# Optimization experiments

Measured on AMD Instinct MI355X. Metric: run time of the kernel, lower is better.

## Reference

```python
import jax, jax.numpy as jnp
from jax import lax
import numpy as np

UNTIL_T = 25  # until_time in source
EPS = 1e-6
K_SEG = 5     # number of temporal groups produced by Segment()


def conv1d(x, w, b=None, padding=((0, 0),)):
    y = lax.conv_general_dilated(x, w, (1,), padding,
                                 dimension_numbers=('NCH', 'OIH', 'NCH'))
    return y if b is None else y + b[None, :, None]


def maxpool1d(x, k, s):
    return lax.reduce_window(x, -jnp.inf, lax.max, (1, 1, k), (1, 1, s), 'VALID')


def batchnorm(x, g, b):
    m = x.mean((0, 2), keepdims=True)
    v = x.var((0, 2), keepdims=True)
    return g[None, :, None] * (x - m) / jnp.sqrt(v + 1e-5) + b[None, :, None]


def miu(x, sign, a, b):
    # fuzzy membership predicate: sigmoid(sign * a_c * (x - b_c))
    return jax.nn.sigmoid(sign * a[None, :, None] * (x - b[None, :, None]))


def upsample2(x):
    B, C, L = x.shape
    return jax.image.resize(x, (B, C, 2 * L), method='linear')


def logic_and(x, w, padding=((0, 0),)):
    # weighted geometric-mean fuzzy AND: exp(conv(log x, softmax(w)))
    wn = jax.nn.softmax(w.reshape(w.shape[0], -1), -1).reshape(w.shape)
    return jax.nn.relu(jnp.exp(conv1d(jnp.log(jnp.clip(x, 0.0, 1.0) + EPS), wn, padding=padding)))


def logic_or(x, w, padding=((0, 0),)):
    # dual fuzzy OR: 1 - exp(conv(log(1-x), softmax(w)))
    wn = jax.nn.softmax(w.reshape(w.shape[0], -1), -1).reshape(w.shape)
    return jax.nn.relu(1.0 - jnp.exp(conv1d(jnp.log(1.0 - jnp.clip(x, 0.0, 1.0) + EPS), wn, padding=padding)))


def until(x, T):
    # Until(x)[t] = max_{1<=d<=T} min( min_{0<=s<d} x[t+s], x[t+d] ), zero right-pad
    L = x.shape[-1]
    xp = jnp.pad(x, ((0, 0), (0, 0), (0, T)))
    runmin = x
    out = jnp.zeros_like(x)  # x >= 0 so 0 is a valid lower bound
    for d in range(1, T + 1):  # small fixed unroll over until_time
        xs = xp[..., d:d + L]
        out = jnp.maximum(out, jnp.minimum(runmin, xs))
        runmin = jnp.minimum(runmin, xs)
    return out[..., :L - 1]  # crop to match kernel-2 logic convs


def forward(x, wave_w, bn_g, bn_b, miu_ap, miu_bp, miu_an, miu_bn,
            ae_w1, ae_b1, ae_w2, ae_b2, ae_w3, ae_b3, ae_w4, ae_b4,
            and2_w, or2_w, and_w, or_w,
            fc1_w, fc1_b, fc2_w, fc2_b, fc3_w, fc3_b):
    B = x.shape[0]
    # Basic predicate network: wavelet conv (k=32) + BN + ReLU + pool -> [B,16,343]
    xf = maxpool1d(jax.nn.relu(batchnorm(conv1d(x, wave_w), bn_g, bn_b)), 3, 2)
    x_pos = maxpool1d(miu(xf, 1.0, miu_ap, miu_bp), 3, 2)    # [B,16,171]
    x_neg = maxpool1d(miu(xf, -1.0, miu_an, miu_bn), 3, 2)   # [B,16,171]
    x_miu = jnp.concatenate([x_pos, x_neg], 1)               # [B,32,171]
    # AutoEncoder -> w, same shape as x_miu
    h = maxpool1d(jnp.tanh(conv1d(x_miu, ae_w1, ae_b1, ((1, 1),))), 3, 2)   # [B,64,85]
    h = maxpool1d(jax.nn.relu(conv1d(h, ae_w2, ae_b2, ((1, 1),))), 3, 2)    # [B,32,42]
    h = jnp.tanh(conv1d(upsample2(h), ae_w3, ae_b3, ((2, 2),)))             # [B,64,86]
    h = jax.nn.sigmoid(conv1d(upsample2(h), ae_w4, ae_b4, ((2, 2),)))       # [B,32,174]
    w = maxpool1d(h, 4, 1)                                                  # [B,32,171]
    # Temporal grouping: K_SEG activation-level bands over w (vectorized, no cat loop)
    lo = (jnp.arange(K_SEG, dtype=w.dtype) / K_SEG)[:, None, None, None]
    hi = (jnp.arange(1, K_SEG + 1, dtype=w.dtype) / K_SEG).at[-1].set(2.0)[:, None, None, None]
    masks = (w[None] >= lo) & (w[None] < hi)                 # [K,B,32,171]
    seg = jnp.where(masks, w[None], 0.0) * x_miu[None]       # select_w * x_miu per segment
    inp = jnp.transpose(seg, (1, 0, 2, 3)).reshape(B, K_SEG * 32, -1)  # [B,160,171]
    x_until = until(inp, UNTIL_T)                            # [B,160,170]
    x_and1 = logic_and(inp, and2_w)                          # [B,20,170]
    x_or1 = logic_or(inp, or2_w)                             # [B,20,170]
    x1 = jnp.concatenate([x_and1, x_or1, x_until], 1)        # [B,200,170]
    x_and2 = logic_and(x1, and_w, ((1, 0),))                 # causal same-pad -> [B,6,170]
    x_or2 = logic_or(x1, or_w, ((1, 0),))                    # [B,6,170]
    x2 = jnp.concatenate([x_and2, x_or2], 1)                 # [B,12,170]
    # Classifier (dropout = identity at inference), Linear over last dim (=170)
    h = jax.nn.relu(jnp.einsum('bcl,ol->bco', x2, fc1_w) + fc1_b)
    h = jax.nn.relu(jnp.einsum('bco,po->bcp', h, fc2_w) + fc2_b)
    return jnp.einsum('bcp,qp->bcq', h, fc3_w) + fc3_b       # [B,12,10]


def setup_inputs() -> dict:
    key = jax.random.key(0)
    ks = jax.random.split(key, 24)
    n = lambda k, shp, s: jax.random.normal(k, shp, jnp.float32) * s
    B = 128
    d = {
        'x': n(ks[0], (B, 1, 719), 1.0),
        'wave_w': n(ks[1], (16, 1, 32), 1.0 / np.sqrt(32)),
        'bn_g': jnp.ones((16,), jnp.float32),
        'bn_b': jnp.zeros((16,), jnp.float32),
        'miu_ap': 1.0 + n(ks[2], (16,), 0.1),
        'miu_bp': n(ks[3], (16,), 0.1),
        'miu_an': 1.0 + n(ks[4], (16,), 0.1),
        'miu_bn': n(ks[5], (16,), 0.1),
        'ae_w1': n(ks[6], (64, 32, 3), 1.0 / np.sqrt(96)),
        'ae_b1': jnp.zeros((64,), jnp.float32),
        'ae_w2': n(ks[7], (32, 64, 3), 1.0 / np.sqrt(192)),
        'ae_b2': jnp.zeros((32,), jnp.float32),
        'ae_w3': n(ks[8], (64, 32, 3), 1.0 / np.sqrt(96)),
        'ae_b3': jnp.zeros((64,), jnp.float32),
        'ae_w4': n(ks[9], (32, 64, 3), 1.0 / np.sqrt(192)),
        'ae_b4': jnp.zeros((32,), jnp.float32),
        'and2_w': n(ks[10], (20, 160, 2), 1.0),
        'or2_w': n(ks[11], (20, 160, 2), 1.0),
        'and_w': n(ks[12], (6, 200, 2), 1.0),
        'or_w': n(ks[13], (6, 200, 2), 1.0),
        'fc1_w': n(ks[14], (1024, 170), 1.0 / np.sqrt(170)),
        'fc1_b': jnp.zeros((1024,), jnp.float32),
        'fc2_w': n(ks[15], (256, 1024), 1.0 / np.sqrt(1024)),
        'fc2_b': jnp.zeros((256,), jnp.float32),
        'fc3_w': n(ks[16], (10, 256), 1.0 / np.sqrt(256)),
        'fc3_b': jnp.zeros((10,), jnp.float32),
    }
    return d


def reference(x, wave_w, bn_g, bn_b, miu_ap, miu_bp, miu_an, miu_bn,
              ae_w1, ae_b1, ae_w2, ae_b2, ae_w3, ae_b3, ae_w4, ae_b4,
              and2_w, or2_w, and_w, or_w,
              fc1_w, fc1_b, fc2_w, fc2_b, fc3_w, fc3_b):
    return forward(x, wave_w, bn_g, bn_b, miu_ap, miu_bp, miu_an, miu_bn,
                   ae_w1, ae_b1, ae_w2, ae_b2, ae_w3, ae_b3, ae_w4, ae_b4,
                   and2_w, or2_w, and_w, or_w,
                   fc1_w, fc1_b, fc2_w, fc2_b, fc3_w, fc3_b)
```

## Files before the change

### kernel.cpp

```cpp
#include <hip/hip_runtime.h>

#define TPB 256
static inline int cdiv(int a, int b){ return (a + b - 1) / b; }

#define EPSL 1e-6f
#define ACT_TANH 0
#define ACT_RELU 1
#define ACT_SIG  2
#define ACT_NONE 3

__device__ __forceinline__ float sigf(float x){ return 1.0f / (1.0f + __expf(-x)); }
__device__ __forceinline__ float clip01(float x){ return fminf(fmaxf(x, 0.f), 1.f); }

#define OFF_Y1   0
#define OFF_XF   1409024
#define OFF_XMIU 2111488
#define OFF_H1   2811904
#define OFF_INP  4384768
#define OFF_X1   7886848
#define OFF_TAIL 12238848
#define OFF_P1   0
#define OFF_P2   (OFF_INP + 400000)
#define OFF_GP   0
#define OFF_X2P  OFF_INP
#define OFF_FC1H OFF_X1
#define OFF_BNP  (OFF_TAIL + 64)
#define OFF_WN   (OFF_TAIL + 64 + 512)
#define OFF_W1P  (OFF_TAIL + 64 + 512 + 17600)

__global__ void __launch_bounds__(TPB) k_misc(const float* __restrict__ a2, const float* __restrict__ o2,
                     const float* __restrict__ aw, const float* __restrict__ ow,
                     float* __restrict__ wn,
                     const float* __restrict__ x, const float* __restrict__ ww,
                     float* __restrict__ y,
                     const float* __restrict__ w1, float* __restrict__ wp){
  int bid = blockIdx.x;
  if (bid < 52){
    const float* src; float* dst; int n;
    if (bid < 20)      { src = a2 + bid*320;      dst = wn + bid*320;              n = 320; }
    else if (bid < 40) { src = o2 + (bid-20)*320; dst = wn + 6400 + (bid-20)*320;  n = 320; }
    else if (bid < 46) { src = aw + (bid-40)*400; dst = wn + 12800 + (bid-40)*400; n = 400; }
    else               { src = ow + (bid-46)*400; dst = wn + 15200 + (bid-46)*400; n = 400; }
    __shared__ float sh[TPB];
    float m = -1e30f;
    for (int i = threadIdx.x; i < n; i += TPB) m = fmaxf(m, src[i]);
    sh[threadIdx.x] = m; __syncthreads();
    for (int off = TPB/2; off > 0; off >>= 1){
      if (threadIdx.x < off) sh[threadIdx.x] = fmaxf(sh[threadIdx.x], sh[threadIdx.x+off]);
      __syncthreads();
    }
    m = sh[0]; __syncthreads();
    float s = 0.f;
    for (int i = threadIdx.x; i < n; i += TPB) s += expf(src[i] - m);
    sh[threadIdx.x] = s; __syncthreads();
    for (int off = TPB/2; off > 0; off >>= 1){
      if (threadIdx.x < off) sh[threadIdx.x] += sh[threadIdx.x+off];
      __syncthreads();
    }
    float inv = 1.0f / sh[0];
    __syncthreads();
    for (int i = threadIdx.x; i < n; i += TPB) dst[i] = expf(src[i] - m) * inv;
  } else if (bid < 52 + 5504){
    int idx = (bid - 52)*TPB + threadIdx.x;
    int l = idx % 688; int t = idx / 688; int o = t & 15; int b = t >> 4;
    const float* xr = x + b*719 + l;
    const float* wr = ww + o*32;
    float s = 0.f;
    #pragma unroll
    for (int k = 0; k < 32; k++) s = fmaf(xr[k], wr[k], s);
    y[idx] = s;
  } else {
    int idx = (bid - 5556)*TPB + threadIdx.x;
    int k = idx % 192; int o = idx / 192;
    wp[idx] = (k < 170) ? w1[o*170 + k] : 0.f;
  }
}

__global__ void k_bn_part(const float* __restrict__ y, double* __restrict__ bnp){
  int c = blockIdx.x & 15, ch = blockIdx.x >> 4;
  double s = 0.0, s2 = 0.0;
  for (int i = threadIdx.x; i < 16*688; i += TPB){
    int b = ch*16 + i/688, l = i % 688;
    float v = y[(b*16 + c)*688 + l];
    s += (double)v; s2 += (double)v * (double)v;
  }
  __shared__ double sh[TPB], sh2[TPB];
  sh[threadIdx.x] = s; sh2[threadIdx.x] = s2; __syncthreads();
  for (int off = TPB/2; off > 0; off >>= 1){
    if (threadIdx.x < off){ sh[threadIdx.x] += sh[threadIdx.x+off]; sh2[threadIdx.x] += sh2[threadIdx.x+off]; }
    __syncthreads();
  }
  if (threadIdx.x == 0){ bnp[blockIdx.x] = sh[0]; bnp[128 + blockIdx.x] = sh2[0]; }
}

__global__ void k_xmiu2(const float* __restrict__ y, const double* __restrict__ bnp,
                        const float* __restrict__ g, const float* __restrict__ bb,
                        const float* __restrict__ ap, const float* __restrict__ bp,
                        const float* __restrict__ an, const float* __restrict__ bn,
                        float* __restrict__ out){
  __shared__ float smean[16], srstd[16];
  if (threadIdx.x < 16){
    int cc = threadIdx.x;
    double s = 0.0, s2 = 0.0;
    #pragma unroll
    for (int j = 0; j < 8; j++){ s += bnp[j*16 + cc]; s2 += bnp[128 + j*16 + cc]; }
    double n = 128.0*688.0;
    double m = s / n;
    double var = s2 / n - m*m;
    smean[cc] = (float)m;
    srstd[cc] = (float)(1.0 / sqrt(var + 1e-5));
  }
  __syncthreads();
  int idx = blockIdx.x*blockDim.x + threadIdx.x;
  if (idx >= 128*32*171) return;
  int l = idx % 171; int t = idx / 171; int c = t & 31; int b = t >> 5;
  int cc = c & 15;
  float mean = smean[cc], rstd = srstd[cc];
  float gc = g[cc], bc = bb[cc];
  float sign = (c < 16) ? 1.f : -1.f;
  float a  = (c < 16) ? ap[cc] : an[cc];
  float bo = (c < 16) ? bp[cc] : bn[cc];
  const float* yr = y + (b*16 + cc)*688 + 4*l;
  float v[7];
  #pragma unroll
  for (int i = 0; i < 7; i++)
    v[i] = fmaxf(fmaf(gc*(yr[i] - mean), rstd, bc), 0.f);
  float m = -1e30f;
  #pragma unroll
  for (int j = 0; j < 3; j++){
    float xf = fmaxf(fmaxf(v[2*j], v[2*j+1]), v[2*j+2]);
    m = fmaxf(m, sigf(sign * a * (xf - bo)));
  }
  out[idx] = m;
}

template<int SMODE, int LSRC, int LEFF>
__device__ __forceinline__ float stage_val(const float* __restrict__ src, int q){
  if (q < 0 || q >= LEFF) return 0.f;
  if constexpr (SMODE == 0){
    return src[q];
  } else if constexpr (SMODE == 1){
    float m = fmaxf(fmaxf(src[2*q], src[2*q+1]), src[2*q+2]);
    return tanhf(m);
  } else if constexpr (SMODE == 2){
    auto P = [&](int k){
      float m = fmaxf(fmaxf(src[2*k], src[2*k+1]), src[2*k+2]);
      return fmaxf(m, 0.f);
    };
    if (q == 0) return P(0);
    if (q == LEFF - 1) return P(LEFF/2 - 1);
    int k = q >> 1;
    return (q & 1) ? 0.75f*P(k) + 0.25f*P(k+1) : 0.25f*P(k-1) + 0.75f*P(k);
  } else {
    if (q == 0) return src[0];
    if (q == LEFF - 1) return src[LSRC - 1];
    int k = q >> 1;
    return (q & 1) ? 0.75f*src[k] + 0.25f*src[k+1] : 0.25f*src[k-1] + 0.75f*src[k];
  }
}

template<int CIN, int LSRC, int LEFF, int COUT, int LOUT, int PAD, int ACT, int PL, int SMODE>
__global__ void __launch_bounds__(256) k_conv(const float* __restrict__ in,
                                              const float* __restrict__ w,
                                              const float* __restrict__ bias,
                                              float* __restrict__ outp){
  constexpr int LSEG = 4*PL;
  constexpr int WL = ((LSEG + 2) + 3) & ~3;
  constexpr int K3 = CIN*3;
  __shared__ float smem[CIN*WL + 8 + K3*COUT];
  float* sin = smem;
  float* wT  = smem + CIN*WL + 8;
  const int b = blockIdx.x;
  const int tid = threadIdx.x;
  const int base = blockIdx.y*LSEG - PAD;

  const float* gin = in + b*CIN*LSRC;
  for (int e = tid; e < CIN*WL; e += 256){
    int i = e / WL, c = e - i*WL;
    sin[e] = stage_val<SMODE, LSRC, LEFF>(gin + i*LSRC, base + c);
  }
  if (tid < 8) sin[CIN*WL + tid] = 0.f;
  for (int e = tid; e < K3*COUT; e += 256){
    int o = e & (COUT-1), m = e / COUT;
    wT[m*COUT + o] = w[o*K3 + m];
  }
  __syncthreads();

  const int to = tid / PL, tp = tid - (tid/PL)*PL;
  const int o0 = to*4;
  const int pl0 = 4*tp;
  float acc[4][4] = {{0,0,0,0},{0,0,0,0},{0,0,0,0},{0,0,0,0}};

  for (int i = 0; i < CIN; i++){
    const float* srow = sin + i*WL + pl0;
    float xv[6];
    *(float4*)&xv[0] = *(const float4*)srow;
    *(float2*)&xv[4] = *(const float2*)(srow + 4);
    const float* wrow = wT + (i*3)*COUT + o0;
    float wv[3][4];
    #pragma unroll
    for (int k = 0; k < 3; k++)
      *(float4*)&wv[k][0] = *(const float4*)(wrow + k*COUT);
    #pragma unroll
    for (int j = 0; j < 4; j++)
      #pragma unroll
      for (int k = 0; k < 3; k++)
        #pragma unroll
        for (int oo = 0; oo < 4; oo++)
          acc[j][oo] = fmaf(xv[j+k], wv[k][oo], acc[j][oo]);
  }

  const int pg0 = blockIdx.y*LSEG + pl0;
  float bv[4];
  #pragma unroll
  for (int oo = 0; oo < 4; oo++) bv[oo] = bias[o0 + oo];
  #pragma unroll
  for (int oo = 0; oo < 4; oo++){
    float* orow = outp + (b*COUT + o0 + oo)*LOUT;
    #pragma unroll
    for (int j = 0; j < 4; j++){
      int p = pg0 + j;
      if (p < LOUT){
        float s = acc[j][oo] + bv[oo];
        float r;
        if (ACT == ACT_TANH)      r = tanhf(s);
        else if (ACT == ACT_RELU) r = fmaxf(s, 0.f);
        else if (ACT == ACT_SIG)  r = sigf(s);
        else                      r = s;
        orow[p] = r;
      }
    }
  }
}

__global__ void k_inp(const float* __restrict__ h4, const float* __restrict__ xmiu,
                      float* __restrict__ inp){
  int idx = blockIdx.x*blockDim.x + threadIdx.x;
  if (idx >= 128*32*171) return;
  int l = idx % 171; int t = idx / 171; int c = t & 31; int b = t >> 5;
  const float* hr = h4 + t*174 + l;
  float wv = fmaxf(fmaxf(hr[0], hr[1]), fmaxf(hr[2], hr[3]));
  float xm = xmiu[idx];
  float prod = wv * xm;
  const float lo[5] = {0.0f, 0.2f, 0.4f, 0.6f, 0.8f};
  const float hi[5] = {0.2f, 0.4f, 0.6f, 0.8f, 2.0f};
  float* op = inp + ((b*160) + c)*171 + l;
  #pragma unroll
  for (int s = 0; s < 5; s++){
    bool m = (wv >= lo[s]) && (wv < hi[s]);
    op[s*32*171] = m ? prod : 0.f;
  }
}

__global__ void __launch_bounds__(TPB) k_ul1(const float* __restrict__ inp, const float* __restrict__ wn,
                                             float* __restrict__ x1, float* __restrict__ p1){
  int bid = blockIdx.x;
  if (bid < 680){
    int xb = bid % 85; int rr = bid / 85; int ch = rr & 3; int v = rr >> 2;
    int bl = xb*TPB + threadIdx.x;
    int l = bl % 170; int b = bl / 170;
    const float* W = wn + (v ? 6400 : 0);
    float acc[20];
    #pragma unroll
    for (int o = 0; o < 20; o++) acc[o] = 0.f;
    int c0 = ch*40;
    const float* ir = inp + (b*160 + c0)*171 + l;
    for (int c = 0; c < 40; c++){
      float u0 = clip01(ir[0]);
      float u1 = clip01(ir[1]);
      float g0, g1;
      if (v){ g0 = __logf(1.f - u0 + EPSL); g1 = __logf(1.f - u1 + EPSL); }
      else  { g0 = __logf(u0 + EPSL);       g1 = __logf(u1 + EPSL); }
      const float* wc = W + 2*(c0 + c);
      #pragma unroll
      for (int o = 0; o < 20; o++)
        acc[o] = fmaf(wc[o*320], g0, fmaf(wc[o*320 + 1], g1, acc[o]));
      ir += 171;
    }
    float* pp = p1 + ((ch*128 + b)*40 + v*20)*170 + l;
    #pragma unroll
    for (int o = 0; o < 20; o++) pp[o*170] = acc[o];
  } else {
    int idx = (bid - 680)*TPB + threadIdx.x;
    int lh = idx % 85; int t = idx / 85; int c = t % 160; int b = t / 160;
    int l0 = 2*lh;
    const float* xr = inp + (b*160 + c)*171;
    float v[27];
    #pragma unroll
    for (int i = 0; i < 27; i++){
      int q = l0 + i;
      v[i] = (q < 171) ? xr[q] : 0.f;
    }
    float rm0 = v[0], o0 = 0.f;
    float rm1 = v[1], o1 = 0.f;
    #pragma unroll
    for (int d = 1; d <= 25; d++){
      o0 = fmaxf(o0, fminf(rm0, v[d]));     rm0 = fminf(rm0, v[d]);
      o1 = fmaxf(o1, fminf(rm1, v[d+1]));   rm1 = fminf(rm1, v[d+1]);
    }
    float2 ov = {o0, o1};
    *(float2*)&x1[((b*200) + 40 + c)*170 + l0] = ov;
  }
}

__global__ void __launch_bounds__(TPB) k_logic2p(const float* __restrict__ x1, const float* __restrict__ p1,
                                                 const float* __restrict__ wn, float* __restrict__ p2){
  int bl = blockIdx.x*TPB + threadIdx.x;
  int l = bl % 170; int b = bl / 170;
  int ch = blockIdx.y, v = blockIdx.z;
  const float* W = wn + 12800 + (v ? 2400 : 0);
  float acc[6] = {0.f,0.f,0.f,0.f,0.f,0.f};
  int c0 = ch*25;
  bool have0 = (l > 0);
  for (int c = c0; c < c0 + 25; c++){
    float u0 = 0.f, u1;
    if (c < 40){
      float s1 = 0.f;
      #pragma unroll
      for (int q = 0; q < 4; q++) s1 += p1[((q*128 + b)*40 + c)*170 + l];
      float e = __expf(s1);
      u1 = (c < 20) ? e : fmaxf(0.f, 1.f - e);
      if (have0){
        float s0 = 0.f;
        #pragma unroll
        for (int q = 0; q < 4; q++) s0 += p1[((q*128 + b)*40 + c)*170 + l - 1];
        float e0 = __expf(s0);
        u0 = (c < 20) ? e0 : fmaxf(0.f, 1.f - e0);
      }
    } else {
      const float* xr = x1 + (b*200 + c)*170 + l;
      u1 = xr[0];
      if (have0) u0 = xr[-1];
    }
    float g0 = 0.f;
    if (have0){
      float uc = clip01(u0);
      g0 = v ? __logf(1.f - uc + EPSL) : __logf(uc + EPSL);
    }
    float uc1 = clip01(u1);
    float g1 = v ? __logf(1.f - uc1 + EPSL) : __logf(uc1 + EPSL);
    const float* wc = W + 2*c;
    #pragma unroll
    for (int o = 0; o < 6; o++)
      acc[o] = fmaf(wc[o*400], g0, fmaf(wc[o*400 + 1], g1, acc[o]));
  }
  float* pp = p2 + ((ch*128 + b)*12 + v*6)*170 + l;
  #pragma unroll
  for (int o = 0; o < 6; o++) pp[o*170] = acc[o];
}

__global__ void k_fin2(const float* __restrict__ p2, float* __restrict__ x2p){
  int idx = blockIdx.x*blockDim.x + threadIdx.x;
  if (idx >= 128*12*192) return;
  int l = idx % 192; int ro = idx / 192;
  if (l >= 170){ x2p[ro*192 + l] = 0.f; return; }
  int o = ro % 12; int b = ro / 12;
  float s = 0.f;
  #pragma unroll
  for (int ch = 0; ch < 8; ch++) s += p2[((ch*128 + b)*12 + o)*170 + l];
  float e = __expf(s);
  float r = (o < 6) ? e : fmaxf(0.f, 1.f - e);
  x2p[ro*192 + l] = r;
}

template<int M, int N, int K, int KSPLIT, int ACT>
__global__ void __launch_bounds__(256) k_gemm(const float* __restrict__ A,
                                              const float* __restrict__ W,
                                              const float* __restrict__ bias,
                                              float* __restrict__ C){
  static_assert(K % (KSPLIT*32) == 0, "K split");
  constexpr int KC = K / KSPLIT;
  constexpr int NT = KC / 32;
  constexpr int S = 68;
  __shared__ float As[2][32*S];
  __shared__ float Bs[2][32*S];
  const int m0 = blockIdx.x*64, n0 = blockIdx.y*64;
  const int kbeg = blockIdx.z*KC;
  const int tid = threadIdx.x;
  const int row = tid >> 2;
  const int c4  = (tid & 3)*4;
  const int tm  = (tid & 15)*4;
  const int tn  = (tid >> 4)*4;

  const float* Ar = A + (m0 + row)*K + kbeg + c4;
  const float* Wr = W + (n0 + row)*K + kbeg + c4;

  float4 ra0 = *(const float4*)(Ar);
  float4 ra1 = *(const float4*)(Ar + 16);
  float4 rb0 = *(const float4*)(Wr);
  float4 rb1 = *(const float4*)(Wr + 16);

  float acc[4][4] = {{0,0,0,0},{0,0,0,0},{0,0,0,0},{0,0,0,0}};
  int buf = 0;
  {
    float* a = As[0]; float* b = Bs[0];
    #pragma unroll
    for (int i = 0; i < 4; i++){
      a[(c4 + i)*S + row]      = ((const float*)&ra0)[i];
      a[(c4 + 16 + i)*S + row] = ((const float*)&ra1)[i];
      b[(c4 + i)*S + row]      = ((const float*)&rb0)[i];
      b[(c4 + 16 + i)*S + row] = ((const float*)&rb1)[i];
    }
  }
  __syncthreads();

  for (int t = 0; t < NT; t++){
    if (t + 1 < NT){
      Ar += 32; Wr += 32;
      ra0 = *(const float4*)(Ar);
      ra1 = *(const float4*)(Ar + 16);
      rb0 = *(const float4*)(Wr);
      rb1 = *(const float4*)(Wr + 16);
    }
    const float* a = As[buf]; const float* b = Bs[buf];
    #pragma unroll
    for (int k = 0; k < 32; k++){
      const float4 av = *(const float4*)(a + k*S + tm);
      const float4 bv = *(const float4*)(b + k*S + tn);
      acc[0][0] = fmaf(av.x, bv.x, acc[0][0]); acc[0][1] = fmaf(av.x, bv.y, acc[0][1]);
      acc[0][2] = fmaf(av.x, bv.z, acc[0][2]); acc[0][3] = fmaf(av.x, bv.w, acc[0][3]);
      acc[1][0] = fmaf(av.y, bv.x, acc[1][0]); acc[1][1] = fmaf(av.y, bv.y, acc[1][1]);
      acc[1][2] = fmaf(av.y, bv.z, acc[1][2]); acc[1][3] = fmaf(av.y, bv.w, acc[1][3]);
      acc[2][0] = fmaf(av.z, bv.x, acc[2][0]); acc[2][1] = fmaf(av.z, bv.y, acc[2][1]);
      acc[2][2] = fmaf(av.z, bv.z, acc[2][2]); acc[2][3] = fmaf(av.z, bv.w, acc[2][3]);
      acc[3][0] = fmaf(av.w, bv.x, acc[3][0]); acc[3][1] = fmaf(av.w, bv.y, acc[3][1]);
      acc[3][2] = fmaf(av.w, bv.z, acc[3][2]); acc[3][3] = fmaf(av.w, bv.w, acc[3][3]);
    }
    if (t + 1 < NT){
      int nb = buf ^ 1;
      float* an = As[nb]; float* bn = Bs[nb];
      #pragma unroll
      for (int i = 0; i < 4; i++){
        an[(c4 + i)*S + row]      = ((const float*)&ra0)[i];
        an[(c4 + 16 + i)*S + row] = ((const float*)&ra1)[i];
        bn[(c4 + i)*S + row]      = ((const float*)&rb0)[i];
        bn[(c4 + 16 + i)*S + row] = ((const float*)&rb1)[i];
      }
      __syncthreads();
      buf = nb;
    }
  }

  if (KSPLIT == 1){
    #pragma unroll
    for (int i = 0; i < 4; i++){
      float4 vv;
      vv.x = acc[i][0] + bias[n0 + tn];
      vv.y = acc[i][1] + bias[n0 + tn + 1];
      vv.z = acc[i][2] + bias[n0 + tn + 2];
      vv.w = acc[i][3] + bias[n0 + tn + 3];
      if (ACT == ACT_RELU){
        vv.x = fmaxf(vv.x, 0.f); vv.y = fmaxf(vv.y, 0.f);
        vv.z = fmaxf(vv.z, 0.f); vv.w = fmaxf(vv.w, 0.f);
      }
      *(float4*)&C[(m0 + tm + i)*N + n0 + tn] = vv;
    }
  } else {
    float* Cz = C + (size_t)blockIdx.z*M*N;
    #pragma unroll
    for (int i = 0; i < 4; i++){
      float4 vv = {acc[i][0], acc[i][1], acc[i][2], acc[i][3]};
      *(float4*)&Cz[(m0 + tm + i)*N + n0 + tn] = vv;
    }
  }
}

__global__ void __launch_bounds__(256) k_tail(const float* __restrict__ gp,
                                              const float* __restrict__ b2,
                                              const float* __restrict__ w3,
                                              const float* __restrict__ b3,
                                              float* __restrict__ out){
  constexpr int MN = 1536*256;
  __shared__ float sh[256];
  __shared__ float ps[160];
  const int row = blockIdx.x;
  const int t = threadIdx.x;
  float s = b2[t];
  #pragma unroll
  for (int z = 0; z < 4; z++) s += gp[(size_t)z*MN + row*256 + t];
  sh[t] = fmaxf(s, 0.f);
  __syncthreads();
  if (t < 160){
    int q = t >> 4, j = t & 15;
    const float* wr = w3 + q*256 + j*16;
    const float* hr = sh + j*16;
    float p = 0.f;
    #pragma unroll
    for (int i = 0; i < 16; i++) p = fmaf(hr[i], wr[i], p);
    ps[t] = p;
  }
  __syncthreads();
  if (t < 10){
    float s3 = b3[t];
    #pragma unroll
    for (int j = 0; j < 16; j++) s3 += ps[t*16 + j];
    out[row*10 + t] = s3;
  }
}

extern "C" void kernel_launch(void* const* d_in, const int* in_sizes, int n_in,
                              void* d_out, int out_size, void* d_ws, size_t ws_size,
                              hipStream_t stream) {
  const float* x      = (const float*)d_in[0];
  const float* wave_w = (const float*)d_in[1];
  const float* bn_g   = (const float*)d_in[2];
  const float* bn_b   = (const float*)d_in[3];
  const float* miu_ap = (const float*)d_in[4];
  const float* miu_bp = (const float*)d_in[5];
  const float* miu_an = (const float*)d_in[6];
  const float* miu_bn = (const float*)d_in[7];
  const float* ae_w1  = (const float*)d_in[8];
  const float* ae_b1  = (const float*)d_in[9];
  const float* ae_w2  = (const float*)d_in[10];
  const float* ae_b2  = (const float*)d_in[11];
  const float* ae_w3  = (const float*)d_in[12];
  const float* ae_b3  = (const float*)d_in[13];
  const float* ae_w4  = (const float*)d_in[14];
  const float* ae_b4  = (const float*)d_in[15];
  const float* and2_w = (const float*)d_in[16];
  const float* or2_w  = (const float*)d_in[17];
  const float* and_w  = (const float*)d_in[18];
  const float* or_w   = (const float*)d_in[19];
  const float* fc1_w  = (const float*)d_in[20];
  const float* fc1_b  = (const float*)d_in[21];
  const float* fc2_w  = (const float*)d_in[22];
  const float* fc2_b  = (const float*)d_in[23];
  const float* fc3_w  = (const float*)d_in[24];
  const float* fc3_b  = (const float*)d_in[25];
  float* out = (float*)d_out;
  float* ws  = (float*)d_ws;

  float* y1    = ws + OFF_Y1;
  float* xmiu  = ws + OFF_XMIU;
  float* c1    = ws + OFF_H1;
  float* c2    = ws + OFF_XF;
  float* h3    = ws + OFF_Y1;
  float* h4    = ws + OFF_H1;
  float* inp   = ws + OFF_INP;
  float* x1    = ws + OFF_X1;
  float* p1    = ws + OFF_P1;
  float* p2    = ws + OFF_P2;
  float* gp    = ws + OFF_GP;
  float* x2p   = ws + OFF_X2P;
  float* w1p   = ws + OFF_W1P;
  float* fc1h  = ws + OFF_FC1H;
  double* bnp  = (double*)(ws + OFF_BNP);
  float* wn    = ws + OFF_WN;

  k_misc     <<<52 + 5504 + 768, TPB, 0, stream>>>(and2_w, or2_w, and_w, or_w, wn,
                                                   x, wave_w, y1, fc1_w, w1p);
  k_bn_part  <<<128, TPB, 0, stream>>>(y1, bnp);
  k_xmiu2    <<<cdiv(128*32*171, TPB), TPB, 0, stream>>>(y1, bnp, bn_g, bn_b,
                                                         miu_ap, miu_bp, miu_an, miu_bn, xmiu);

  k_conv<32,171,171,64,171,1,ACT_NONE,16,0><<<dim3(128,3), 256, 0, stream>>>(xmiu, ae_w1, ae_b1, c1);
  k_conv<64,171, 85,32, 85,1,ACT_NONE,32,1><<<dim3(128,1), 256, 0, stream>>>(c1, ae_w2, ae_b2, c2);
  k_conv<32, 85, 84,64, 86,2,ACT_TANH,16,2><<<dim3(128,2), 256, 0, stream>>>(c2, ae_w3, ae_b3, h3);
  k_conv<64, 86,172,32,174,2,ACT_SIG ,32,3><<<dim3(128,2), 256, 0, stream>>>(h3, ae_w4, ae_b4, h4);

  k_inp      <<<cdiv(128*32*171, TPB), TPB, 0, stream>>>(h4, xmiu, inp);
  k_ul1      <<<680 + 6800, TPB, 0, stream>>>(inp, wn, x1, p1);
  k_logic2p  <<<dim3(85, 8, 2), TPB, 0, stream>>>(x1, p1, wn, p2);
  k_fin2     <<<cdiv(128*12*192, TPB), TPB, 0, stream>>>(p2, x2p);

  k_gemm<1536,1024,192,1,ACT_RELU><<<dim3(24,16,1), 256, 0, stream>>>(x2p, w1p, fc1_b, fc1h);
  k_gemm<1536,256,1024,4,ACT_NONE><<<dim3(24,4,4), 256, 0, stream>>>(fc1h, fc2_w, fc2_b, gp);
  k_tail     <<<1536, 256, 0, stream>>>(gp, fc2_b, fc3_w, fc3_b, out);
}
```

Before: 317.2 us.

## Split reductions and conv tiles finer to raise grid parallelism across kernels

Doubles the block count for the batchnorm partial sums, and splits the fuzzy-AND/OR channel reduction into eight chunks instead of four, moving the p1 buffer to a new offset so it fits. Adds a per-thread output-tile template parameter to the conv kernel so the two 32-output-channel convs use 2-wide tiles with more blocks. Makes the until kernel compute four outputs per thread so the 25-step window loads are shared. The aim is better GPU occupancy for small grids, at the cost of more partial-sum traffic and scalar shared-memory loads in place of vector loads.

Result: faster. 297.7 us (-6.1%).

```diff
diff --git a/kernel.cpp b/kernel.cpp
--- a/kernel.cpp
+++ b/kernel.cpp
@@ -19,14 +19,14 @@
 #define OFF_INP  4384768
 #define OFF_X1   7886848
 #define OFF_TAIL 12238848
-#define OFF_P1   0
 #define OFF_P2   (OFF_INP + 400000)
 #define OFF_GP   0
 #define OFF_X2P  OFF_INP
 #define OFF_FC1H OFF_X1
 #define OFF_BNP  (OFF_TAIL + 64)
-#define OFF_WN   (OFF_TAIL + 64 + 512)
-#define OFF_W1P  (OFF_TAIL + 64 + 512 + 17600)
+#define OFF_WN   (OFF_TAIL + 64 + 1024)
+#define OFF_W1P  (OFF_TAIL + 64 + 1024 + 17600)
+#define OFF_P1   16000000
 
 __global__ void __launch_bounds__(TPB) k_misc(const float* __restrict__ a2, const float* __restrict__ o2,
                      const float* __restrict__ aw, const float* __restrict__ ow,
@@ -79,8 +79,8 @@
 __global__ void k_bn_part(const float* __restrict__ y, double* __restrict__ bnp){
   int c = blockIdx.x & 15, ch = blockIdx.x >> 4;
   double s = 0.0, s2 = 0.0;
-  for (int i = threadIdx.x; i < 16*688; i += TPB){
-    int b = ch*16 + i/688, l = i % 688;
+  for (int i = threadIdx.x; i < 8*688; i += TPB){
+    int b = ch*8 + i/688, l = i % 688;
     float v = y[(b*16 + c)*688 + l];
     s += (double)v; s2 += (double)v * (double)v;
   }
@@ -90,7 +90,7 @@
     if (threadIdx.x < off){ sh[threadIdx.x] += sh[threadIdx.x+off]; sh2[threadIdx.x] += sh2[threadIdx.x+off]; }
     __syncthreads();
   }
-  if (threadIdx.x == 0){ bnp[blockIdx.x] = sh[0]; bnp[128 + blockIdx.x] = sh2[0]; }
+  if (threadIdx.x == 0){ bnp[blockIdx.x] = sh[0]; bnp[256 + blockIdx.x] = sh2[0]; }
 }
 
 __global__ void k_xmiu2(const float* __restrict__ y, const double* __restrict__ bnp,
@@ -103,7 +103,7 @@
     int cc = threadIdx.x;
     double s = 0.0, s2 = 0.0;
     #pragma unroll
-    for (int j = 0; j < 8; j++){ s += bnp[j*16 + cc]; s2 += bnp[128 + j*16 + cc]; }
+    for (int j = 0; j < 16; j++){ s += bnp[j*16 + cc]; s2 += bnp[256 + j*16 + cc]; }
     double n = 128.0*688.0;
     double m = s / n;
     double var = s2 / n - m*m;
@@ -159,12 +159,12 @@
   }
 }
 
-template<int CIN, int LSRC, int LEFF, int COUT, int LOUT, int PAD, int ACT, int PL, int SMODE>
+template<int CIN, int LSRC, int LEFF, int COUT, int LOUT, int PAD, int ACT, int PL, int SMODE, int JT>
 __global__ void __launch_bounds__(256) k_conv(const float* __restrict__ in,
                                               const float* __restrict__ w,
                                               const float* __restrict__ bias,
                                               float* __restrict__ outp){
-  constexpr int LSEG = 4*PL;
+  constexpr int LSEG = JT*PL;
   constexpr int WL = ((LSEG + 2) + 3) & ~3;
   constexpr int K3 = CIN*3;
   __shared__ float smem[CIN*WL + 8 + K3*COUT];
@@ -188,21 +188,25 @@
 
   const int to = tid / PL, tp = tid - (tid/PL)*PL;
   const int o0 = to*4;
-  const int pl0 = 4*tp;
-  float acc[4][4] = {{0,0,0,0},{0,0,0,0},{0,0,0,0},{0,0,0,0}};
+  const int pl0 = JT*tp;
+  float acc[JT][4];
+  #pragma unroll
+  for (int j = 0; j < JT; j++)
+    #pragma unroll
+    for (int oo = 0; oo < 4; oo++) acc[j][oo] = 0.f;
 
   for (int i = 0; i < CIN; i++){
     const float* srow = sin + i*WL + pl0;
-    float xv[6];
-    *(float4*)&xv[0] = *(const float4*)srow;
-    *(float2*)&xv[4] = *(const float2*)(srow + 4);
+    float xv[JT+2];
+    #pragma unroll
+    for (int j = 0; j < JT+2; j++) xv[j] = srow[j];
     const float* wrow = wT + (i*3)*COUT + o0;
     float wv[3][4];
     #pragma unroll
     for (int k = 0; k < 3; k++)
       *(float4*)&wv[k][0] = *(const float4*)(wrow + k*COUT);
     #pragma unroll
-    for (int j = 0; j < 4; j++)
+    for (int j = 0; j < JT; j++)
       #pragma unroll
       for (int k = 0; k < 3; k++)
         #pragma unroll
@@ -218,7 +222,7 @@
   for (int oo = 0; oo < 4; oo++){
     float* orow = outp + (b*COUT + o0 + oo)*LOUT;
     #pragma unroll
-    for (int j = 0; j < 4; j++){
+    for (int j = 0; j < JT; j++){
       int p = pg0 + j;
       if (p < LOUT){
         float s = acc[j][oo] + bv[oo];
@@ -255,17 +259,17 @@
 __global__ void __launch_bounds__(TPB) k_ul1(const float* __restrict__ inp, const float* __restrict__ wn,
                                              float* __restrict__ x1, float* __restrict__ p1){
   int bid = blockIdx.x;
-  if (bid < 680){
-    int xb = bid % 85; int rr = bid / 85; int ch = rr & 3; int v = rr >> 2;
+  if (bid < 1360){
+    int xb = bid % 85; int rr = bid / 85; int ch = rr & 7; int v = rr >> 3;
     int bl = xb*TPB + threadIdx.x;
     int l = bl % 170; int b = bl / 170;
     const float* W = wn + (v ? 6400 : 0);
     float acc[20];
     #pragma unroll
     for (int o = 0; o < 20; o++) acc[o] = 0.f;
-    int c0 = ch*40;
+    int c0 = ch*20;
     const float* ir = inp + (b*160 + c0)*171 + l;
-    for (int c = 0; c < 40; c++){
+    for (int c = 0; c < 20; c++){
       float u0 = clip01(ir[0]);
       float u1 = clip01(ir[1]);
       float g0, g1;
@@ -281,25 +285,30 @@
     #pragma unroll
     for (int o = 0; o < 20; o++) pp[o*170] = acc[o];
   } else {
-    int idx = (bid - 680)*TPB + threadIdx.x;
-    int lh = idx % 85; int t = idx / 85; int c = t % 160; int b = t / 160;
-    int l0 = 2*lh;
+    int idx = (bid - 1360)*TPB + threadIdx.x;
+    int lh = idx % 43; int t = idx / 43; int c = t % 160; int b = t / 160;
+    int l0 = 4*lh;
     const float* xr = inp + (b*160 + c)*171;
-    float v[27];
-    #pragma unroll
-    for (int i = 0; i < 27; i++){
+    float v[29];
+    #pragma unroll
+    for (int i = 0; i < 29; i++){
       int q = l0 + i;
       v[i] = (q < 171) ? xr[q] : 0.f;
     }
     float rm0 = v[0], o0 = 0.f;
     float rm1 = v[1], o1 = 0.f;
+    float rm2 = v[2], o2 = 0.f;
+    float rm3 = v[3], o3 = 0.f;
     #pragma unroll
     for (int d = 1; d <= 25; d++){
       o0 = fmaxf(o0, fminf(rm0, v[d]));     rm0 = fminf(rm0, v[d]);
       o1 = fmaxf(o1, fminf(rm1, v[d+1]));   rm1 = fminf(rm1, v[d+1]);
-    }
-    float2 ov = {o0, o1};
-    *(float2*)&x1[((b*200) + 40 + c)*170 + l0] = ov;
+      o2 = fmaxf(o2, fminf(rm2, v[d+2]));   rm2 = fminf(rm2, v[d+2]);
+      o3 = fmaxf(o3, fminf(rm3, v[d+3]));   rm3 = fminf(rm3, v[d+3]);
+    }
+    float* xw = x1 + ((b*200) + 40 + c)*170;
+    if (l0 + 1 < 170){ float2 ov = {o0, o1}; *(float2*)&xw[l0] = ov; }
+    if (l0 + 3 < 170){ float2 ov = {o2, o3}; *(float2*)&xw[l0 + 2] = ov; }
   }
 }
 
@@ -317,13 +326,13 @@
     if (c < 40){
       float s1 = 0.f;
       #pragma unroll
-      for (int q = 0; q < 4; q++) s1 += p1[((q*128 + b)*40 + c)*170 + l];
+      for (int q = 0; q < 8; q++) s1 += p1[((q*128 + b)*40 + c)*170 + l];
       float e = __expf(s1);
       u1 = (c < 20) ? e : fmaxf(0.f, 1.f - e);
       if (have0){
         float s0 = 0.f;
         #pragma unroll
-        for (int q = 0; q < 4; q++) s0 += p1[((q*128 + b)*40 + c)*170 + l - 1];
+        for (int q = 0; q < 8; q++) s0 += p1[((q*128 + b)*40 + c)*170 + l - 1];
         float e0 = __expf(s0);
         u0 = (c < 20) ? e0 : fmaxf(0.f, 1.f - e0);
       }
@@ -549,17 +558,17 @@
 
   k_misc     <<<52 + 5504 + 768, TPB, 0, stream>>>(and2_w, or2_w, and_w, or_w, wn,
                                                    x, wave_w, y1, fc1_w, w1p);
-  k_bn_part  <<<128, TPB, 0, stream>>>(y1, bnp);
+  k_bn_part  <<<256, TPB, 0, stream>>>(y1, bnp);
   k_xmiu2    <<<cdiv(128*32*171, TPB), TPB, 0, stream>>>(y1, bnp, bn_g, bn_b,
                                                          miu_ap, miu_bp, miu_an, miu_bn, xmiu);
 
-  k_conv<32,171,171,64,171,1,ACT_NONE,16,0><<<dim3(128,3), 256, 0, stream>>>(xmiu, ae_w1, ae_b1, c1);
-  k_conv<64,171, 85,32, 85,1,ACT_NONE,32,1><<<dim3(128,1), 256, 0, stream>>>(c1, ae_w2, ae_b2, c2);
-  k_conv<32, 85, 84,64, 86,2,ACT_TANH,16,2><<<dim3(128,2), 256, 0, stream>>>(c2, ae_w3, ae_b3, h3);
-  k_conv<64, 86,172,32,174,2,ACT_SIG ,32,3><<<dim3(128,2), 256, 0, stream>>>(h3, ae_w4, ae_b4, h4);
+  k_conv<32,171,171,64,171,1,ACT_NONE,16,0,4><<<dim3(128,3), 256, 0, stream>>>(xmiu, ae_w1, ae_b1, c1);
+  k_conv<64,171, 85,32, 85,1,ACT_NONE,32,1,2><<<dim3(128,2), 256, 0, stream>>>(c1, ae_w2, ae_b2, c2);
+  k_conv<32, 85, 84,64, 86,2,ACT_TANH,16,2,4><<<dim3(128,2), 256, 0, stream>>>(c2, ae_w3, ae_b3, h3);
+  k_conv<64, 86,172,32,174,2,ACT_SIG ,32,3,2><<<dim3(128,3), 256, 0, stream>>>(h3, ae_w4, ae_b4, h4);
 
   k_inp      <<<cdiv(128*32*171, TPB), TPB, 0, stream>>>(h4, xmiu, inp);
-  k_ul1      <<<680 + 6800, TPB, 0, stream>>>(inp, wn, x1, p1);
+  k_ul1      <<<1360 + 3440, TPB, 0, stream>>>(inp, wn, x1, p1);
   k_logic2p  <<<dim3(85, 8, 2), TPB, 0, stream>>>(x1, p1, wn, p2);
   k_fin2     <<<cdiv(128*12*192, TPB), TPB, 0, stream>>>(p2, x2p);
 
```
